# Performance work log

Measured on AMD Instinct MI355X. Metric: run time of the kernel, lower is better.

## Reference

```python
import jax, jax.numpy as jnp
import numpy as np

NEG_SLOPE = 0.2  # PyG GATConv default LeakyReLU slope
EPS = 1e-16      # PyG softmax denominator epsilon


def _gat_layer(x, src, dst, W, a_src, a_dst, b, H, C):
    """One PyG-style GATConv layer (eval mode, add_self_loops already applied).
    x: [N, F_in], W: [F_in, H*C], a_src/a_dst: [H, C], b: [H*C]."""
    N = x.shape[0]
    h = (x @ W).reshape(N, H, C)                       # [N,H,C]
    alpha_src = jnp.sum(h * a_src, axis=-1)            # [N,H]
    alpha_dst = jnp.sum(h * a_dst, axis=-1)            # [N,H]
    e = jax.nn.leaky_relu(alpha_src[src] + alpha_dst[dst], NEG_SLOPE)  # [E,H]
    m = jax.ops.segment_max(e, dst, num_segments=N)    # [N,H] segment-softmax max
    p = jnp.exp(e - m[dst])                            # [E,H]
    s = jax.ops.segment_sum(p, dst, num_segments=N)    # [N,H]
    attn = p / (s[dst] + EPS)                          # [E,H]
    out = jax.ops.segment_sum(attn[:, :, None] * h[src], dst, num_segments=N)  # [N,H,C]
    return out.reshape(N, H * C) + b


def _add_self_loops(edge_index, N):
    loop = jnp.arange(N, dtype=edge_index.dtype)
    src = jnp.concatenate([edge_index[0], loop])
    dst = jnp.concatenate([edge_index[1], loop])
    return src, dst


def setup_inputs() -> dict:
    key = jax.random.key(0)
    N, E = 50000, 500000
    F_in, H, C = 336, 4, 128
    HC = H * C  # 512
    n_cls = 10
    ks = jax.random.split(key, 16)

    def glorot(k, shape):
        fan = shape[0] + shape[-1]
        return jax.random.normal(k, shape, jnp.float32) * jnp.sqrt(2.0 / fan)

    x = jax.random.normal(ks[0], (N, F_in), jnp.float32)
    edge_index = jax.random.randint(ks[1], (2, E), 0, N, dtype=jnp.int64)
    return {
        "x": x,
        "edge_index": edge_index,
        "W1": glorot(ks[2], (F_in, HC)),
        "a_src1": glorot(ks[3], (H, C)),
        "a_dst1": glorot(ks[4], (H, C)),
        "b1": jnp.zeros((HC,), jnp.float32),
        "W2": glorot(ks[5], (HC, HC)),
        "a_src2": glorot(ks[6], (H, C)),
        "a_dst2": glorot(ks[7], (H, C)),
        "b2": jnp.zeros((HC,), jnp.float32),
        "Wc1": glorot(ks[8], (HC, C)),
        "bc1": jnp.zeros((C,), jnp.float32),
        "Wc2": glorot(ks[9], (C, n_cls)),
        "bc2": jnp.zeros((n_cls,), jnp.float32),
    }


def reference(x, edge_index, W1, a_src1, a_dst1, b1, W2, a_src2, a_dst2, b2, Wc1, bc1, Wc2, bc2):
    H, C = 4, 128
    N = x.shape[0]
    src, dst = _add_self_loops(edge_index, N)
    h = _gat_layer(x, src, dst, W1, a_src1, a_dst1, b1, H, C)
    h = jax.nn.elu(h)  # ELU between layers only
    h = _gat_layer(h, src, dst, W2, a_src2, a_dst2, b2, H, C)
    # classifier (dropout is identity in eval)
    z = jax.nn.relu(h @ Wc1 + bc1)
    logits = z @ Wc2 + bc2
    return logits
```

## Files before the change

kernel.cpp:

```cpp
#include <hip/hip_runtime.h>
#include <math.h>

typedef unsigned short u16;
typedef unsigned int u32;
typedef short short8 __attribute__((ext_vector_type(8)));
typedef __bf16 bf16x8 __attribute__((ext_vector_type(8)));
typedef float f32x4 __attribute__((ext_vector_type(4)));

__device__ __forceinline__ float b2f(u16 u) {
    union { u32 i; float f; } v; v.i = ((u32)u) << 16; return v.f;
}
__device__ __forceinline__ float b2f_lo(u32 q) {
    union { u32 i; float f; } v; v.i = q << 16; return v.f;
}
__device__ __forceinline__ float b2f_hi(u32 q) {
    union { u32 i; float f; } v; v.i = q & 0xffff0000u; return v.f;
}
__device__ __forceinline__ u16 f2b(float f) {
    union { float f; u32 i; } v; v.f = f;
    u32 i = v.i;
    u32 r = (i + 0x7fffu + ((i >> 16) & 1u)) >> 16;
    return (u16)r;
}
__device__ __forceinline__ u32 pack2(u16 a, u16 b) { return (u32)a | ((u32)b << 16); }


__device__ void agg_dev(const int* __restrict__ rowptr, const int* __restrict__ col,
                        const float* __restrict__ asrc, const float* __restrict__ adst,
                        const u16* __restrict__ hb, const float* __restrict__ bias,
                        u16* __restrict__ outb, int elu, int NODES) {
    const int wid = (blockIdx.x * 256 + threadIdx.x) >> 6;
    const int nwaves = gridDim.x << 2;
    const int l = threadIdx.x & 63;
    const int hd = l >> 4;
    const int cbase = 8 * l;
    float bv[8];
#pragma unroll
    for (int c = 0; c < 8; c++) bv[c] = bias[cbase + c];

    for (int n = wid; n < NODES; n += nwaves) {
        int beg = rowptr[n], end = rowptr[n + 1];
        float ad = adst[n * 4 + hd];
        float acc0[8], acc1[8];
#pragma unroll
        for (int c = 0; c < 8; c++) { acc0[c] = 0.f; acc1[c] = 0.f; }
        float ss0 = 0.f, ss1 = 0.f;
        int j = beg;
        for (; j + 3 < end; j += 4) {
            int s0 = col[j], s1 = col[j + 1], s2 = col[j + 2], s3 = col[j + 3];
            const u32* hp0 = (const u32*)(hb + (size_t)s0 * 512 + cbase);
            const u32* hp1 = (const u32*)(hb + (size_t)s1 * 512 + cbase);
            const u32* hp2 = (const u32*)(hb + (size_t)s2 * 512 + cbase);
            const u32* hp3 = (const u32*)(hb + (size_t)s3 * 512 + cbase);
            u32 q00 = hp0[0], q01 = hp0[1], q02 = hp0[2], q03 = hp0[3];
            u32 q10 = hp1[0], q11 = hp1[1], q12 = hp1[2], q13 = hp1[3];
            u32 q20 = hp2[0], q21 = hp2[1], q22 = hp2[2], q23 = hp2[3];
            u32 q30 = hp3[0], q31 = hp3[1], q32 = hp3[2], q33 = hp3[3];
            float e0 = asrc[s0 * 4 + hd] + ad; e0 = e0 > 0.f ? e0 : 0.2f * e0;
            float e1 = asrc[s1 * 4 + hd] + ad; e1 = e1 > 0.f ? e1 : 0.2f * e1;
            float e2 = asrc[s2 * 4 + hd] + ad; e2 = e2 > 0.f ? e2 : 0.2f * e2;
            float e3 = asrc[s3 * 4 + hd] + ad; e3 = e3 > 0.f ? e3 : 0.2f * e3;
            float p0 = __expf(e0), p1 = __expf(e1), p2 = __expf(e2), p3 = __expf(e3);
            ss0 += p0 + p2; ss1 += p1 + p3;
            acc0[0] += p0 * b2f_lo(q00) + p2 * b2f_lo(q20);
            acc0[1] += p0 * b2f_hi(q00) + p2 * b2f_hi(q20);
            acc0[2] += p0 * b2f_lo(q01) + p2 * b2f_lo(q21);
            acc0[3] += p0 * b2f_hi(q01) + p2 * b2f_hi(q21);
            acc0[4] += p0 * b2f_lo(q02) + p2 * b2f_lo(q22);
            acc0[5] += p0 * b2f_hi(q02) + p2 * b2f_hi(q22);
            acc0[6] += p0 * b2f_lo(q03) + p2 * b2f_lo(q23);
            acc0[7] += p0 * b2f_hi(q03) + p2 * b2f_hi(q23);
            acc1[0] += p1 * b2f_lo(q10) + p3 * b2f_lo(q30);
            acc1[1] += p1 * b2f_hi(q10) + p3 * b2f_hi(q30);
            acc1[2] += p1 * b2f_lo(q11) + p3 * b2f_lo(q31);
            acc1[3] += p1 * b2f_hi(q11) + p3 * b2f_hi(q31);
            acc1[4] += p1 * b2f_lo(q12) + p3 * b2f_lo(q32);
            acc1[5] += p1 * b2f_hi(q12) + p3 * b2f_hi(q32);
            acc1[6] += p1 * b2f_lo(q13) + p3 * b2f_lo(q33);
            acc1[7] += p1 * b2f_hi(q13) + p3 * b2f_hi(q33);
        }
        for (; j < end; ++j) {
            int s0 = col[j];
            const u32* hp0 = (const u32*)(hb + (size_t)s0 * 512 + cbase);
            u32 q00 = hp0[0], q01 = hp0[1], q02 = hp0[2], q03 = hp0[3];
            float e0 = asrc[s0 * 4 + hd] + ad; e0 = e0 > 0.f ? e0 : 0.2f * e0;
            float p0 = __expf(e0);
            ss0 += p0;
            acc0[0] += p0 * b2f_lo(q00); acc0[1] += p0 * b2f_hi(q00);
            acc0[2] += p0 * b2f_lo(q01); acc0[3] += p0 * b2f_hi(q01);
            acc0[4] += p0 * b2f_lo(q02); acc0[5] += p0 * b2f_hi(q02);
            acc0[6] += p0 * b2f_lo(q03); acc0[7] += p0 * b2f_hi(q03);
        }
        float inv = 1.f / (ss0 + ss1 + 1e-16f);
        float v[8];
#pragma unroll
        for (int c = 0; c < 8; c++) {
            float tv = (acc0[c] + acc1[c]) * inv + bv[c];
            if (elu) tv = tv > 0.f ? tv : expm1f(tv);
            v[c] = tv;
        }
        u32* op = (u32*)(outb + (size_t)n * 512 + cbase);
        op[0] = pack2(f2b(v[0]), f2b(v[1]));
        op[1] = pack2(f2b(v[2]), f2b(v[3]));
        op[2] = pack2(f2b(v[4]), f2b(v[5]));
        op[3] = pack2(f2b(v[6]), f2b(v[7]));
    }
}

__device__ void gemm_dev(const u16* __restrict__ A, const u16* __restrict__ Bt,
                         u16* __restrict__ C, const float* __restrict__ bias,
                         const float* __restrict__ aS, const float* __restrict__ aD,
                         float* __restrict__ asr, float* __restrict__ ads,
                         const float* __restrict__ Wc2, const float* __restrict__ bc2,
                         float* __restrict__ outp,
                         int M, int N, int K, int act, char* shm,
                         u16* As, u16* Bs, float (*red)[128][2]) {
    const int t = threadIdx.x;
    const int l = t & 63, w = t >> 6;
    const int m0 = blockIdx.x * 128, n0 = blockIdx.y * 128;
    const int sr = t >> 2;
    const int sc = (t & 3) * 8;
    const int wm = (w >> 1) * 64, wn = (w & 1) * 64;

    const int rA0 = min(m0 + sr, M - 1);
    const int rA1 = min(m0 + sr + 64, M - 1);
    const int rB0 = min(n0 + sr, N - 1);
    const int rB1 = min(n0 + sr + 64, N - 1);

    f32x4 acc[4][4];
    f32x4 z4 = {0.f, 0.f, 0.f, 0.f};
#pragma unroll
    for (int i = 0; i < 4; i++)
#pragma unroll
        for (int j = 0; j < 4; j++) acc[i][j] = z4;

    for (int k0 = 0; k0 < K; k0 += 32) {
        short8 a0 = *(const short8*)(A + (size_t)rA0 * K + k0 + sc);
        short8 a1 = *(const short8*)(A + (size_t)rA1 * K + k0 + sc);
        short8 b0 = *(const short8*)(Bt + (size_t)rB0 * K + k0 + sc);
        short8 b1 = *(const short8*)(Bt + (size_t)rB1 * K + k0 + sc);
        __syncthreads();
        *(short8*)(As + sr * 32 + sc) = a0;
        *(short8*)(As + (sr + 64) * 32 + sc) = a1;
        *(short8*)(Bs + sr * 32 + sc) = b0;
        *(short8*)(Bs + (sr + 64) * 32 + sc) = b1;
        __syncthreads();

        bf16x8 af[4], bfr[4];
#pragma unroll
        for (int i = 0; i < 4; i++) {
            af[i]  = *(const bf16x8*)(As + (wm + i * 16 + (l & 15)) * 32 + (l >> 4) * 8);
            bfr[i] = *(const bf16x8*)(Bs + (wn + i * 16 + (l & 15)) * 32 + (l >> 4) * 8);
        }
#pragma unroll
        for (int i = 0; i < 4; i++)
#pragma unroll
            for (int j = 0; j < 4; j++)
                acc[i][j] = __builtin_amdgcn_mfma_f32_16x16x32_bf16(af[i], bfr[j], acc[i][j], 0, 0, 0);
    }

    if (act == 2) {
        __syncthreads();
        float* wl = (float*)shm;
        float (*logbuf)[128][10] = (float (*)[128][10])(shm + 8192);
        for (int i = t; i < 1280; i += 256) wl[i] = Wc2[i];
        if (t < 10) wl[1280 + t] = bc2[t];
        __syncthreads();
        float aSv[4];
        int cj[4];
#pragma unroll
        for (int j = 0; j < 4; j++) cj[j] = wn + j * 16 + (l & 15);
        (void)aSv;
#pragma unroll
        for (int i = 0; i < 4; i++) {
#pragma unroll
            for (int r = 0; r < 4; r++) {
                float zv[4];
#pragma unroll
                for (int j = 0; j < 4; j++) {
                    float v = acc[i][j][r] + (bias ? bias[cj[j]] : 0.f);
                    zv[j] = v > 0.f ? v : 0.f;
                }
                float part[10];
#pragma unroll
                for (int k = 0; k < 10; k++) {
                    float s = 0.f;
#pragma unroll
                    for (int j = 0; j < 4; j++) s += zv[j] * wl[cj[j] * 10 + k];
#pragma unroll
                    for (int o = 1; o < 16; o <<= 1) s += __shfl_xor(s, o);
                    part[k] = s;
                }
                if ((l & 15) == 0) {
                    int rl = wm + i * 16 + (l >> 4) * 4 + r;
#pragma unroll
                    for (int k = 0; k < 10; k++) logbuf[w & 1][rl][k] = part[k];
                }
            }
        }
        __syncthreads();
        if (t < 128) {
            int row = m0 + t;
            if (row < M) {
#pragma unroll
                for (int k = 0; k < 10; k++)
                    outp[(size_t)row * 10 + k] =
                        logbuf[0][t][k] + logbuf[1][t][k] + wl[1280 + k];
            }
        }
        return;
    }

#pragma unroll
    for (int i = 0; i < 4; i++) {
        int rbase = m0 + wm + i * 16 + (l >> 4) * 4;
#pragma unroll
        for (int j = 0; j < 4; j++) {
            int c = n0 + wn + j * 16 + (l & 15);
            float bv = bias ? bias[c] : 0.f;
#pragma unroll
            for (int r = 0; r < 4; r++) {
                int row = rbase + r;
                if (row < M) {
                    float v = acc[i][j][r] + bv;
                    if (act == 1) v = v > 0.f ? v : 0.f;
                    C[(size_t)row * N + c] = f2b(v);
                }
            }
        }
    }

    if (aS) {
        const int hd = n0 >> 7;
        float aSv[4], aDv[4];
#pragma unroll
        for (int j = 0; j < 4; j++) {
            int c = n0 + wn + j * 16 + (l & 15);
            aSv[j] = aS[c];
            aDv[j] = aD[c];
        }
#pragma unroll
        for (int i = 0; i < 4; i++) {
#pragma unroll
            for (int r = 0; r < 4; r++) {
                float vs = 0.f, vd = 0.f;
#pragma unroll
                for (int j = 0; j < 4; j++) {
                    float hv = acc[i][j][r];
                    vs += hv * aSv[j];
                    vd += hv * aDv[j];
                }
#pragma unroll
                for (int o = 1; o < 16; o <<= 1) {
                    vs += __shfl_xor(vs, o);
                    vd += __shfl_xor(vd, o);
                }
                if ((l & 15) == 0) {
                    int rl = wm + i * 16 + (l >> 4) * 4 + r;
                    red[w & 1][rl][0] = vs;
                    red[w & 1][rl][1] = vd;
                }
            }
        }
        __syncthreads();
        if (t < 128) {
            int row = m0 + t;
            if (row < M) {
                asr[row * 4 + hd] = red[0][t][0] + red[1][t][0];
                ads[row * 4 + hd] = red[0][t][1] + red[1][t][1];
            }
        }
    }
}

__global__ __launch_bounds__(256) void BaselineGAT_41764261987077_kernel(
    int phase, int aux,
    const float* x, const int* ei,
    const float* W1, const float* as1, const float* ad1, const float* b1,
    const float* W2, const float* as2, const float* ad2, const float* b2,
    const float* Wc1, const float* bc1, const float* Wc2, const float* bc2,
    float* out,
    u16* hAb, u16* hbB, float* asr, float* ads,
    u16* xb, u16* w1t, u16* w2t, u16* wc1t,
    int* flag, int* cnt, int* tmp, int* bsum, int* boff,
    int* rowptr, int* cursor, int* col,
    const u16* gA, const u16* gB, u16* gC, const float* gBias,
    const float* gAs, const float* gAd,
    int gM, int gN, int gK, int gAct,
    int NODES, int E, int nblk)
{
    __shared__ f32x4 shm4[1156];
    char* shm = (char*)shm4;
    u16* As = (u16*)shm;
    u16* Bs = (u16*)(shm + 8192);
    float (*red)[128][2] = (float (*)[128][2])(shm + 16384);
    float* smf = (float*)shm;
    int* smi = (int*)shm;

    const int t = threadIdx.x;
    const int gid = blockIdx.x * 256 + t;
    const int EN = E + NODES;

    switch (phase) {
    case 100: {
        float v = (aux == 0) ? 0.25f : 1000.0f;
        if (gid < NODES * 10) out[gid] = v;
    } break;
    case 0: {
        if (blockIdx.x == 0) {
            if (t == 0) smi[256] = 0;
            __syncthreads();
            for (int j = t; j < 1024; j += 256)
                if (ei[2 * j + 1] != 0) atomicAdd(&smi[256], 1);
            __syncthreads();
            if (t == 0) flag[0] = (smi[256] < 16) ? 2 : 1;
        } else {
            int i = (blockIdx.x - 1) * 256 + t;
            if (i < NODES) cnt[i] = 0;
        }
    } break;
    case 2: {
        if (gid >= EN) return;
        int step = flag[0];
        int d;
        if (gid < E) {
            d = ei[(size_t)(E + gid) * step];
            if ((unsigned)d >= (unsigned)NODES) d = 0;
        } else d = gid - E;
        atomicAdd(&cnt[d], 1);
    } break;
    case 3: {
        smi[t] = (gid < NODES) ? cnt[gid] : 0;
        __syncthreads();
        for (int o = 1; o < 256; o <<= 1) {
            int add = (t >= o) ? smi[t - o] : 0;
            __syncthreads();
            smi[t] += add;
            __syncthreads();
        }
        if (gid < NODES) tmp[gid] = smi[t];
        if (t == 255) bsum[blockIdx.x] = smi[255];
    } break;
    case 4: {
        if (blockIdx.x == 0 && t == 0) {
            int ex = 0;
            for (int b = 0; b < nblk; b++) { boff[b] = ex; ex += bsum[b]; }
        }
    } break;
    case 5: {
        if (gid >= NODES) return;
        int incl = tmp[gid] + boff[blockIdx.x];
        rowptr[gid + 1] = incl;
        cursor[gid] = incl - cnt[gid];
        if (gid == 0) rowptr[0] = 0;
    } break;
    case 6: {
        if (gid >= EN) return;
        int step = flag[0];
        int d, s;
        if (gid < E) {
            s = ei[(size_t)gid * step];
            d = ei[(size_t)(E + gid) * step];
            if ((unsigned)s >= (unsigned)NODES) s = 0;
            if ((unsigned)d >= (unsigned)NODES) d = 0;
        } else { d = gid - E; s = d; }
        int pos = atomicAdd(&cursor[d], 1);
        col[pos] = s;
    } break;
    case 20: {
        int i = gid;
        const int XC = NODES * 44;
        if (i < XC) {
            int n = i / 44, kk = (i - n * 44) * 8;
            short8 o;
            if (kk < 336) {
                const f32x4* xp = (const f32x4*)(x + (size_t)n * 336 + kk);
                f32x4 f0 = xp[0], f1 = xp[1];
                o[0] = (short)f2b(f0[0]); o[1] = (short)f2b(f0[1]);
                o[2] = (short)f2b(f0[2]); o[3] = (short)f2b(f0[3]);
                o[4] = (short)f2b(f1[0]); o[5] = (short)f2b(f1[1]);
                o[6] = (short)f2b(f1[2]); o[7] = (short)f2b(f1[3]);
            } else {
#pragma unroll
                for (int e = 0; e < 8; e++) o[e] = 0;
            }
            *(short8*)(xb + (size_t)n * 352 + kk) = o;
            return;
        }
        i -= XC;
        if (i < 512 * 352) {
            int n = i / 352, k = i - n * 352;
            w1t[i] = (k < 336) ? f2b(W1[(size_t)k * 512 + n]) : (u16)0;
            return;
        }
        i -= 512 * 352;
        if (i < 512 * 512) {
            int n = i >> 9, k = i & 511;
            w2t[i] = f2b(W2[(size_t)k * 512 + n]);
            return;
        }
        i -= 512 * 512;
        if (i < 128 * 512) {
            int n = i >> 9, k = i & 511;
            wc1t[i] = f2b(Wc1[(size_t)k * 128 + n]);
        }
    } break;
    case 30: gemm_dev(gA, gB, gC, gBias, gAs, gAd, asr, ads,
                      Wc2, bc2, out, gM, gN, gK, gAct, shm, As, Bs, red); break;
    case 31: agg_dev(rowptr, col, asr, ads, hAb, gBias, hbB, aux, NODES); break;
    }
}

extern "C" void kernel_launch(void* const* d_in, const int* in_sizes, int n_in,
                              void* d_out, int out_size, void* d_ws, size_t ws_size,
                              hipStream_t stream) {
    const float* x   = (const float*)d_in[0];
    const int*   ei  = (const int*)d_in[1];
    const float* W1  = (const float*)d_in[2];
    const float* as1 = (const float*)d_in[3];
    const float* ad1 = (const float*)d_in[4];
    const float* b1  = (const float*)d_in[5];
    const float* W2  = (const float*)d_in[6];
    const float* as2 = (const float*)d_in[7];
    const float* ad2 = (const float*)d_in[8];
    const float* b2  = (const float*)d_in[9];
    const float* Wc1 = (const float*)d_in[10];
    const float* bc1 = (const float*)d_in[11];
    const float* Wc2 = (const float*)d_in[12];
    const float* bc2 = (const float*)d_in[13];

    const int NODES = in_sizes[0] / 336;
    const int E     = in_sizes[1] / 2;

    char* ws = (char*)d_ws;
    size_t off = 0;
    auto alloc = [&](size_t b) -> char* {
        char* p = ws + off; off = (off + b + 255) & ~(size_t)255; return p;
    };
    u16*   xb   = (u16*)alloc((size_t)NODES * 352 * 2);
    u16*   hAb  = (u16*)alloc((size_t)NODES * 512 * 2);
    u16*   hbB  = (u16*)alloc((size_t)NODES * 512 * 2);
    float* asr  = (float*)alloc((size_t)NODES * 4 * 4);
    float* ads  = (float*)alloc((size_t)NODES * 4 * 4);
    u16*   w1t  = (u16*)alloc((size_t)512 * 352 * 2);
    u16*   w2t  = (u16*)alloc((size_t)512 * 512 * 2);
    u16*   wc1t = (u16*)alloc((size_t)128 * 512 * 2);
    int* flag   = (int*)alloc(256);
    int* cnt    = (int*)alloc((size_t)NODES * 4);
    int* tmp    = (int*)alloc((size_t)NODES * 4);
    int* bsum   = (int*)alloc(4096);
    int* boff   = (int*)alloc(4096);
    int* rowptr = (int*)alloc((size_t)(NODES + 1) * 4);
    int* cursor = (int*)alloc((size_t)NODES * 4);
    int* col    = (int*)alloc((size_t)(E + NODES) * 4);

    const int nblk = (NODES + 255) / 256;
    const int eblk = (E + NODES + 255) / 256;
    const int oblk = (out_size + 255) / 256;
    const int mt   = (NODES + 127) / 128;
    const int cvt_total = NODES * 44 + 512 * 352 + 512 * 512 + 128 * 512;

    auto L = [&](int phase, int aux, dim3 grid,
                 const u16* gA = nullptr, const u16* gB = nullptr,
                 u16* gC = nullptr, const float* gBias = nullptr,
                 const float* gAs = nullptr, const float* gAd = nullptr,
                 int gM = 0, int gN = 0, int gK = 0, int gAct = 0) {
        BaselineGAT_41764261987077_kernel<<<grid, 256, 0, stream>>>(
            phase, aux, x, ei, W1, as1, ad1, b1, W2, as2, ad2, b2,
            Wc1, bc1, Wc2, bc2, (float*)d_out,
            hAb, hbB, asr, ads, xb, w1t, w2t, wc1t,
            flag, cnt, tmp, bsum, boff, rowptr, cursor, col,
            gA, gB, gC, gBias, gAs, gAd, gM, gN, gK, gAct,
            NODES, E, nblk);
    };

    L(100, 0, oblk);
    if (n_in < 14 || off > ws_size) { L(100, 1, oblk); return; }

    L(0, 0, nblk + 1);
    L(2, 0, eblk);
    L(3, 0, nblk);
    L(4, 0, 1);
    L(5, 0, nblk);
    L(6, 0, eblk);

    L(20, 0, (cvt_total + 255) / 256);

    L(30, 0, dim3(mt, 4), xb, w1t, hAb, nullptr, as1, ad1, NODES, 512, 352, 0);
    L(31, 1, 1024, nullptr, nullptr, nullptr, b1);

    L(30, 0, dim3(mt, 4), hbB, w2t, hAb, nullptr, as2, ad2, NODES, 512, 512, 0);
    L(31, 0, 1024, nullptr, nullptr, nullptr, b2);

    L(30, 0, dim3(mt, 1), hbB, wc1t, nullptr, bc1, nullptr, nullptr, NODES, 128, 512, 2);
}
```

Measured before the change: 669.6 us.

## Vectorize gather loads, merge block-offset scan, drop init launch, enlarge aggregation grid

The aggregation kernel now gathers each neighbour's 8 bf16 features with one 128-bit vector load instead of four 32-bit loads. The serial single-thread block-offset scan launch is removed, and each block of the rowptr phase recomputes the prefix over block sums in shared memory. The unconditional output pre-fill launch is dropped, and the aggregation phases launch 4096 blocks instead of 1024. Together these cut launch count and serial latency and raise memory-level parallelism, at the cost of redundant per-block scan work. The redundant scan assumes nblk is at most 256.

```diff
diff --git a/kernel.cpp b/kernel.cpp
--- a/kernel.cpp
+++ b/kernel.cpp
@@ -6,6 +6,7 @@
 typedef short short8 __attribute__((ext_vector_type(8)));
 typedef __bf16 bf16x8 __attribute__((ext_vector_type(8)));
 typedef float f32x4 __attribute__((ext_vector_type(4)));
+typedef u32 u32x4 __attribute__((ext_vector_type(4)));
 
 __device__ __forceinline__ float b2f(u16 u) {
     union { u32 i; float f; } v; v.i = ((u32)u) << 16; return v.f;
@@ -48,48 +49,35 @@
         int j = beg;
         for (; j + 3 < end; j += 4) {
             int s0 = col[j], s1 = col[j + 1], s2 = col[j + 2], s3 = col[j + 3];
-            const u32* hp0 = (const u32*)(hb + (size_t)s0 * 512 + cbase);
-            const u32* hp1 = (const u32*)(hb + (size_t)s1 * 512 + cbase);
-            const u32* hp2 = (const u32*)(hb + (size_t)s2 * 512 + cbase);
-            const u32* hp3 = (const u32*)(hb + (size_t)s3 * 512 + cbase);
-            u32 q00 = hp0[0], q01 = hp0[1], q02 = hp0[2], q03 = hp0[3];
-            u32 q10 = hp1[0], q11 = hp1[1], q12 = hp1[2], q13 = hp1[3];
-            u32 q20 = hp2[0], q21 = hp2[1], q22 = hp2[2], q23 = hp2[3];
-            u32 q30 = hp3[0], q31 = hp3[1], q32 = hp3[2], q33 = hp3[3];
+            u32x4 q0 = *(const u32x4*)(hb + (size_t)s0 * 512 + cbase);
+            u32x4 q1 = *(const u32x4*)(hb + (size_t)s1 * 512 + cbase);
+            u32x4 q2 = *(const u32x4*)(hb + (size_t)s2 * 512 + cbase);
+            u32x4 q3 = *(const u32x4*)(hb + (size_t)s3 * 512 + cbase);
             float e0 = asrc[s0 * 4 + hd] + ad; e0 = e0 > 0.f ? e0 : 0.2f * e0;
             float e1 = asrc[s1 * 4 + hd] + ad; e1 = e1 > 0.f ? e1 : 0.2f * e1;
             float e2 = asrc[s2 * 4 + hd] + ad; e2 = e2 > 0.f ? e2 : 0.2f * e2;
             float e3 = asrc[s3 * 4 + hd] + ad; e3 = e3 > 0.f ? e3 : 0.2f * e3;
             float p0 = __expf(e0), p1 = __expf(e1), p2 = __expf(e2), p3 = __expf(e3);
             ss0 += p0 + p2; ss1 += p1 + p3;
-            acc0[0] += p0 * b2f_lo(q00) + p2 * b2f_lo(q20);
-            acc0[1] += p0 * b2f_hi(q00) + p2 * b2f_hi(q20);
-            acc0[2] += p0 * b2f_lo(q01) + p2 * b2f_lo(q21);
-            acc0[3] += p0 * b2f_hi(q01) + p2 * b2f_hi(q21);
-            acc0[4] += p0 * b2f_lo(q02) + p2 * b2f_lo(q22);
-            acc0[5] += p0 * b2f_hi(q02) + p2 * b2f_hi(q22);
-            acc0[6] += p0 * b2f_lo(q03) + p2 * b2f_lo(q23);
-            acc0[7] += p0 * b2f_hi(q03) + p2 * b2f_hi(q23);
-            acc1[0] += p1 * b2f_lo(q10) + p3 * b2f_lo(q30);
-            acc1[1] += p1 * b2f_hi(q10) + p3 * b2f_hi(q30);
-            acc1[2] += p1 * b2f_lo(q11) + p3 * b2f_lo(q31);
-            acc1[3] += p1 * b2f_hi(q11) + p3 * b2f_hi(q31);
-            acc1[4] += p1 * b2f_lo(q12) + p3 * b2f_lo(q32);
-            acc1[5] += p1 * b2f_hi(q12) + p3 * b2f_hi(q32);
-            acc1[6] += p1 * b2f_lo(q13) + p3 * b2f_lo(q33);
-            acc1[7] += p1 * b2f_hi(q13) + p3 * b2f_hi(q33);
+#pragma unroll
+            for (int q = 0; q < 4; q++) {
+                acc0[2 * q]     += p0 * b2f_lo(q0[q]) + p2 * b2f_lo(q2[q]);
+                acc0[2 * q + 1] += p0 * b2f_hi(q0[q]) + p2 * b2f_hi(q2[q]);
+                acc1[2 * q]     += p1 * b2f_lo(q1[q]) + p3 * b2f_lo(q3[q]);
+                acc1[2 * q + 1] += p1 * b2f_hi(q1[q]) + p3 * b2f_hi(q3[q]);
+            }
         }
         for (; j < end; ++j) {
             int s0 = col[j];
-            const u32* hp0 = (const u32*)(hb + (size_t)s0 * 512 + cbase);
-            u32 q00 = hp0[0], q01 = hp0[1], q02 = hp0[2], q03 = hp0[3];
+            u32x4 q0 = *(const u32x4*)(hb + (size_t)s0 * 512 + cbase);
             float e0 = asrc[s0 * 4 + hd] + ad; e0 = e0 > 0.f ? e0 : 0.2f * e0;
             float p0 = __expf(e0);
             ss0 += p0;
-            acc0[0] += p0 * b2f_lo(q00); acc0[1] += p0 * b2f_hi(q00);
-            acc0[2] += p0 * b2f_lo(q01); acc0[3] += p0 * b2f_hi(q01);
-            acc0[4] += p0 * b2f_lo(q02); acc0[5] += p0 * b2f_hi(q02);
-            acc0[6] += p0 * b2f_lo(q03); acc0[7] += p0 * b2f_hi(q03);
+#pragma unroll
+            for (int q = 0; q < 4; q++) {
+                acc0[2 * q]     += p0 * b2f_lo(q0[q]);
+                acc0[2 * q + 1] += p0 * b2f_hi(q0[q]);
+            }
         }
         float inv = 1.f / (ss0 + ss1 + 1e-16f);
         float v[8];
@@ -166,11 +154,9 @@
         for (int i = t; i < 1280; i += 256) wl[i] = Wc2[i];
         if (t < 10) wl[1280 + t] = bc2[t];
         __syncthreads();
-        float aSv[4];
         int cj[4];
 #pragma unroll
         for (int j = 0; j < 4; j++) cj[j] = wn + j * 16 + (l & 15);
-        (void)aSv;
 #pragma unroll
         for (int i = 0; i < 4; i++) {
 #pragma unroll
@@ -294,8 +280,8 @@
     u16* As = (u16*)shm;
     u16* Bs = (u16*)(shm + 8192);
     float (*red)[128][2] = (float (*)[128][2])(shm + 16384);
-    float* smf = (float*)shm;
     int* smi = (int*)shm;
+    int* smb = (int*)(shm + 2048);
 
     const int t = threadIdx.x;
     const int gid = blockIdx.x * 256 + t;
@@ -303,8 +289,7 @@
 
     switch (phase) {
     case 100: {
-        float v = (aux == 0) ? 0.25f : 1000.0f;
-        if (gid < NODES * 10) out[gid] = v;
+        if (gid < NODES * 10) out[gid] = 1000.0f;
     } break;
     case 0: {
         if (blockIdx.x == 0) {
@@ -341,15 +326,18 @@
         if (gid < NODES) tmp[gid] = smi[t];
         if (t == 255) bsum[blockIdx.x] = smi[255];
     } break;
-    case 4: {
-        if (blockIdx.x == 0 && t == 0) {
-            int ex = 0;
-            for (int b = 0; b < nblk; b++) { boff[b] = ex; ex += bsum[b]; }
-        }
-    } break;
     case 5: {
+        smb[t] = (t < nblk) ? bsum[t] : 0;
+        __syncthreads();
+        for (int o = 1; o < 256; o <<= 1) {
+            int add = (t >= o) ? smb[t - o] : 0;
+            __syncthreads();
+            smb[t] += add;
+            __syncthreads();
+        }
+        int base = (blockIdx.x == 0) ? 0 : smb[blockIdx.x - 1];
         if (gid >= NODES) return;
-        int incl = tmp[gid] + boff[blockIdx.x];
+        int incl = tmp[gid] + base;
         rowptr[gid + 1] = incl;
         cursor[gid] = incl - cnt[gid];
         if (gid == 0) rowptr[0] = 0;
@@ -474,23 +462,21 @@
             NODES, E, nblk);
     };
 
-    L(100, 0, oblk);
     if (n_in < 14 || off > ws_size) { L(100, 1, oblk); return; }
 
     L(0, 0, nblk + 1);
     L(2, 0, eblk);
     L(3, 0, nblk);
-    L(4, 0, 1);
     L(5, 0, nblk);
     L(6, 0, eblk);
 
     L(20, 0, (cvt_total + 255) / 256);
 
     L(30, 0, dim3(mt, 4), xb, w1t, hAb, nullptr, as1, ad1, NODES, 512, 352, 0);
-    L(31, 1, 1024, nullptr, nullptr, nullptr, b1);
+    L(31, 1, 4096, nullptr, nullptr, nullptr, b1);
 
     L(30, 0, dim3(mt, 4), hbB, w2t, hAb, nullptr, as2, ad2, NODES, 512, 512, 0);
-    L(31, 0, 1024, nullptr, nullptr, nullptr, b2);
+    L(31, 0, 4096, nullptr, nullptr, nullptr, b2);
 
     L(30, 0, dim3(mt, 1), hbB, wc1t, nullptr, bc1, nullptr, nullptr, NODES, 128, 512, 2);
 }
```

Result: faster. 652.6 us (-2.5%).
